# Kernel tuning notes

Measured on AMD Instinct MI355X. Metric: run time of the kernel, lower is better.

## Reference

```python
import jax, jax.numpy as jnp
import numpy as np

VOCAB, T, IN, H, L = 32000, 4096, 512, 256, 2


def setup_inputs() -> dict:
    key = jax.random.key(0)
    ks = jax.random.split(key, 32)
    inp = {}
    inp["tokens"] = jax.random.randint(ks[0], (T,), 0, VOCAB)
    inp["emb"] = jax.random.normal(ks[1], (VOCAB, IN), dtype=jnp.float32) * 0.02
    i = 2
    for d in ("f", "b"):
        for l in range(L):
            in_l = IN if l == 0 else H
            inp[f"{d}_Wih{l}"] = jax.random.normal(ks[i], (4 * H, in_l), dtype=jnp.float32) * 0.05; i += 1
            inp[f"{d}_Whh{l}"] = jax.random.normal(ks[i], (4 * H, H), dtype=jnp.float32) * 0.05; i += 1
            inp[f"{d}_bih{l}"] = jnp.zeros((4 * H,), dtype=jnp.float32)
            inp[f"{d}_bhh{l}"] = jnp.zeros((4 * H,), dtype=jnp.float32)
    return inp


def _lstm_layer(x_seq, Wih, Whh, bih, bhh):
    # x_seq: [T, in]; torch.nn.LSTMCell gate order: i, f, g, o
    Hh = Whh.shape[1]
    b = bih + bhh
    def step(carry, x):
        h, c = carry
        g = x @ Wih.T + h @ Whh.T + b           # [4H]
        i_, f_, g_, o_ = jnp.split(g, 4)
        c = jax.nn.sigmoid(f_) * c + jax.nn.sigmoid(i_) * jnp.tanh(g_)
        h = jax.nn.sigmoid(o_) * jnp.tanh(c)
        return (h, c), h
    z = jnp.zeros((Hh,), x_seq.dtype)
    (h, c), hs = jax.lax.scan(step, (z, z), x_seq)
    return hs, h, c                              # [T,H], [H], [H]


def _run_dir(x_seq, params):
    finals = []
    h_seq = x_seq
    for (Wih, Whh, bih, bhh) in params:
        h_seq, h, c = _lstm_layer(h_seq, Wih, Whh, bih, bhh)
        finals.append((c, h))
    return h_seq, finals


def reference(tokens, emb,
              f_Wih0, f_Whh0, f_bih0, f_bhh0, f_Wih1, f_Whh1, f_bih1, f_bhh1,
              b_Wih0, b_Whh0, b_bih0, b_bhh0, b_Wih1, b_Whh1, b_bih1, b_bhh1):
    x = emb[tokens]                              # [T, IN] embedding lookup
    fparams = [(f_Wih0, f_Whh0, f_bih0, f_bhh0), (f_Wih1, f_Whh1, f_bih1, f_bhh1)]
    bparams = [(b_Wih0, b_Whh0, b_bih0, b_bhh0), (b_Wih1, b_Whh1, b_bih1, b_bhh1)]
    f_out, f_fin = _run_dir(x, fparams)          # forward over sequence
    b_out_rev, b_fin = _run_dir(x[::-1], bparams)  # backward over reversed sequence
    b_out = b_out_rev[::-1]
    outputs = jnp.concatenate([f_out, b_out], axis=-1)  # [T, 2H]
    cell_memories = jnp.stack([jnp.stack([f_fin[l][0], b_fin[l][0]]) for l in range(L)])  # [L,2,H]
    hidden_states = jnp.stack([jnp.stack([f_fin[l][1], b_fin[l][1]]) for l in range(L)])  # [L,2,H]
    return cell_memories, hidden_states, outputs
```

## Files before the change

### kernel.cpp

```cpp
#include <hip/hip_runtime.h>
#include <math.h>

#define T_SEQ 4096

__device__ __forceinline__ float sigmoidf_(float x) {
  return 1.0f / (1.0f + expf(-x));
}

__device__ __forceinline__ unsigned long long pack_h(int tag, float h) {
  return ((unsigned long long)(unsigned)tag << 32) |
         (unsigned long long)__float_as_uint(h);
}

__global__ void gather_emb(const int* __restrict__ tokens,
                           const float4* __restrict__ emb4,
                           float4* __restrict__ X4) {
  int i = blockIdx.x * 256 + threadIdx.x;
  int t = i >> 7;
  int q = i & 127;
  X4[i] = emb4[(long)tokens[t] * 128 + q];
}

__global__ __launch_bounds__(256) void gemm_proj(
    const float* __restrict__ Xf, const float* __restrict__ Xb, int revb,
    const float* __restrict__ Wf, const float* __restrict__ Wb,
    const float* __restrict__ bihf, const float* __restrict__ bhhf,
    const float* __restrict__ bihb, const float* __restrict__ bhhb,
    float* __restrict__ Pf, float* __restrict__ Pb, int K)
{
  const int dirb = blockIdx.z;
  const float* X  = dirb ? Xb : Xf;
  const float* W  = dirb ? Wb : Wf;
  const float* bih = dirb ? bihb : bihf;
  const float* bhh = dirb ? bhhb : bhhf;
  float* Pp = dirb ? Pb : Pf;
  const int rev = dirb ? revb : 0;

  const int bn = blockIdx.x;
  const int bm = blockIdx.y;
  const int tid = threadIdx.x;
  const int tx = tid & 15, ty = tid >> 4;

  __shared__ float Xs[16][68];
  __shared__ float Ws[16][68];

  float acc[4][4] = {{0.f}};

  const int lrow = tid >> 2;
  const int lk4  = (tid & 3) * 4;
  const int xrow = bm * 64 + lrow;
  const int xsrc = rev ? (4095 - xrow) : xrow;
  const float* xptr = X + (long)xsrc * K + lk4;
  const float* wptr = W + (long)(bn * 64 + lrow) * K + lk4;

  for (int k0 = 0; k0 < K; k0 += 16) {
    float4 xv = *(const float4*)(xptr + k0);
    float4 wv = *(const float4*)(wptr + k0);
    __syncthreads();
    Xs[lk4 + 0][lrow] = xv.x; Xs[lk4 + 1][lrow] = xv.y;
    Xs[lk4 + 2][lrow] = xv.z; Xs[lk4 + 3][lrow] = xv.w;
    Ws[lk4 + 0][lrow] = wv.x; Ws[lk4 + 1][lrow] = wv.y;
    Ws[lk4 + 2][lrow] = wv.z; Ws[lk4 + 3][lrow] = wv.w;
    __syncthreads();
    #pragma unroll
    for (int kk = 0; kk < 16; ++kk) {
      float4 a = *(const float4*)(&Xs[kk][ty * 4]);
      float4 b = *(const float4*)(&Ws[kk][tx * 4]);
      acc[0][0] = fmaf(a.x, b.x, acc[0][0]); acc[0][1] = fmaf(a.x, b.y, acc[0][1]);
      acc[0][2] = fmaf(a.x, b.z, acc[0][2]); acc[0][3] = fmaf(a.x, b.w, acc[0][3]);
      acc[1][0] = fmaf(a.y, b.x, acc[1][0]); acc[1][1] = fmaf(a.y, b.y, acc[1][1]);
      acc[1][2] = fmaf(a.y, b.z, acc[1][2]); acc[1][3] = fmaf(a.y, b.w, acc[1][3]);
      acc[2][0] = fmaf(a.z, b.x, acc[2][0]); acc[2][1] = fmaf(a.z, b.y, acc[2][1]);
      acc[2][2] = fmaf(a.z, b.z, acc[2][2]); acc[2][3] = fmaf(a.z, b.w, acc[2][3]);
      acc[3][0] = fmaf(a.w, b.x, acc[3][0]); acc[3][1] = fmaf(a.w, b.y, acc[3][1]);
      acc[3][2] = fmaf(a.w, b.z, acc[3][2]); acc[3][3] = fmaf(a.w, b.w, acc[3][3]);
    }
  }

  const int c0 = bn * 64 + tx * 4;
  #pragma unroll
  for (int i = 0; i < 4; ++i) {
    const int r = bm * 64 + ty * 4 + i;
    float4 o4;
    o4.x = acc[i][0] + bih[c0 + 0] + bhh[c0 + 0];
    o4.y = acc[i][1] + bih[c0 + 1] + bhh[c0 + 1];
    o4.z = acc[i][2] + bih[c0 + 2] + bhh[c0 + 2];
    o4.w = acc[i][3] + bih[c0 + 3] + bhh[c0 + 3];
    *(float4*)(&Pp[(long)r * 1024 + c0]) = o4;
  }
}

__global__ __launch_bounds__(512, 2) void lstm_fused(
    const float* __restrict__ P0f, const float* __restrict__ P0b,
    const float* __restrict__ Whh0f, const float* __restrict__ Whh0b,
    const float* __restrict__ Wih1f, const float* __restrict__ Whh1f,
    const float* __restrict__ bih1f, const float* __restrict__ bhh1f,
    const float* __restrict__ Wih1b, const float* __restrict__ Whh1b,
    const float* __restrict__ bih1b, const float* __restrict__ bhh1b,
    float* __restrict__ out,
    unsigned long long* __restrict__ ring0,
    unsigned long long* __restrict__ h1x)
{
  const int bx = blockIdx.x;
  const int t  = threadIdx.x;

  __shared__ float hx[512];
  __shared__ float lds_c[64];
  __shared__ float part[8 * 264];

  if (t < 64) lds_c[t] = 0.0f;

  if (bx < 8) {
    const int d = bx >> 2, w = bx & 3;
    const float* __restrict__ P = d ? P0b : P0f;
    const float* __restrict__ W = d ? Whh0b : Whh0f;
    unsigned long long* ring = ring0 + (long)d * T_SEQ * 256;

    const int kb = t >> 6;
    const int jg = t & 63;

    float wreg[128];
    #pragma unroll
    for (int jj = 0; jj < 4; ++jj) {
      const int m = jg * 4 + jj;
      const int j = (m >> 6) * 256 + w * 64 + (m & 63);
      const float4* wrow = (const float4*)(W + (long)j * 256 + kb * 32);
      #pragma unroll
      for (int kq = 0; kq < 8; ++kq) {
        float4 v = wrow[kq];
        wreg[jj * 32 + kq * 4 + 0] = v.x;
        wreg[jj * 32 + kq * 4 + 1] = v.y;
        wreg[jj * 32 + kq * 4 + 2] = v.z;
        wreg[jj * 32 + kq * 4 + 3] = v.w;
      }
    }

    const int cell = w * 64 + (t & 63);
    const long pbase = (long)(t & 63) + w * 64;

    for (int s = 0; s < T_SEQ; ++s) {
      float p0 = 0.f, p1 = 0.f, p2 = 0.f, p3 = 0.f;
      if (t < 64) {
        const float* prow = P + (long)s * 1024 + pbase;
        p0 = prow[0]; p1 = prow[256]; p2 = prow[512]; p3 = prow[768];
      }

      if (s == 0) {
        if (t < 256) hx[t] = 0.0f;
      } else if (t < 256) {
        const unsigned long long* src = ring + (long)(s - 1) * 256 + t;
        unsigned long long v;
        do {
          v = __hip_atomic_load(src, __ATOMIC_RELAXED, __HIP_MEMORY_SCOPE_AGENT);
        } while ((unsigned)(v >> 32) != (unsigned)s);
        hx[t] = __uint_as_float((unsigned)v);
      }
      __syncthreads();

      float a0 = 0.f, a1 = 0.f, a2 = 0.f, a3 = 0.f;
      const float4* h4 = (const float4*)&hx[kb * 32];
      #pragma unroll
      for (int kq = 0; kq < 8; ++kq) {
        float4 hv = h4[kq];
        a0 = fmaf(wreg[0 * 32 + kq * 4 + 0], hv.x, a0);
        a0 = fmaf(wreg[0 * 32 + kq * 4 + 1], hv.y, a0);
        a0 = fmaf(wreg[0 * 32 + kq * 4 + 2], hv.z, a0);
        a0 = fmaf(wreg[0 * 32 + kq * 4 + 3], hv.w, a0);
        a1 = fmaf(wreg[1 * 32 + kq * 4 + 0], hv.x, a1);
        a1 = fmaf(wreg[1 * 32 + kq * 4 + 1], hv.y, a1);
        a1 = fmaf(wreg[1 * 32 + kq * 4 + 2], hv.z, a1);
        a1 = fmaf(wreg[1 * 32 + kq * 4 + 3], hv.w, a1);
        a2 = fmaf(wreg[2 * 32 + kq * 4 + 0], hv.x, a2);
        a2 = fmaf(wreg[2 * 32 + kq * 4 + 1], hv.y, a2);
        a2 = fmaf(wreg[2 * 32 + kq * 4 + 2], hv.z, a2);
        a2 = fmaf(wreg[2 * 32 + kq * 4 + 3], hv.w, a2);
        a3 = fmaf(wreg[3 * 32 + kq * 4 + 0], hv.x, a3);
        a3 = fmaf(wreg[3 * 32 + kq * 4 + 1], hv.y, a3);
        a3 = fmaf(wreg[3 * 32 + kq * 4 + 2], hv.z, a3);
        a3 = fmaf(wreg[3 * 32 + kq * 4 + 3], hv.w, a3);
      }
      float4 av; av.x = a0; av.y = a1; av.z = a2; av.w = a3;
      *(float4*)(&part[kb * 264 + jg * 4]) = av;
      __syncthreads();

      if (t < 64) {
        float s0 = p0, s1 = p1, s2 = p2, s3 = p3;
        #pragma unroll
        for (int q = 0; q < 8; ++q) {
          s0 += part[q * 264 + t];
          s1 += part[q * 264 + 64 + t];
          s2 += part[q * 264 + 128 + t];
          s3 += part[q * 264 + 192 + t];
        }
        float c = sigmoidf_(s1) * lds_c[t] + sigmoidf_(s0) * tanhf(s2);
        float h = sigmoidf_(s3) * tanhf(c);
        lds_c[t] = c;
        __hip_atomic_store(ring + (long)s * 256 + cell, pack_h(s + 1, h),
                           __ATOMIC_RELAXED, __HIP_MEMORY_SCOPE_AGENT);
        if (s == T_SEQ - 1) {
          out[d * 256 + cell] = c;
          out[1024 + d * 256 + cell] = h;
        }
      }
    }
  } else {
    const int i1 = bx - 8, d = i1 >> 3, w1 = i1 & 7;
    const float* __restrict__ Wih = d ? Wih1b : Wih1f;
    const float* __restrict__ Whh = d ? Whh1b : Whh1f;
    const float* __restrict__ bih = d ? bih1b : bih1f;
    const float* __restrict__ bhh = d ? bhh1b : bhh1f;
    unsigned long long* ring = ring0 + (long)d * T_SEQ * 256;
    unsigned long long* slot = h1x + d * 512;
    float* hout = d ? (out + 2048 + (long)4095 * 512 + 256) : (out + 2048);
    const long hstr = d ? -512 : 512;

    const int kb = t >> 6;
    const int jg = t & 63;

    float wreg[2][64];
    #pragma unroll
    for (int rr = 0; rr < 2; ++rr) {
      const int m = jg * 2 + rr;
      const int j = (m >> 5) * 256 + w1 * 32 + (m & 31);
      const float* srcw = (kb < 4) ? (Wih + (long)j * 256 + kb * 64)
                                   : (Whh + (long)j * 256 + (kb - 4) * 64);
      const float4* s4 = (const float4*)srcw;
      #pragma unroll
      for (int q = 0; q < 16; ++q) {
        float4 v = s4[q];
        wreg[rr][q * 4 + 0] = v.x; wreg[rr][q * 4 + 1] = v.y;
        wreg[rr][q * 4 + 2] = v.z; wreg[rr][q * 4 + 3] = v.w;
      }
    }

    const int cell = w1 * 32 + (t & 31);
    float b0 = 0.f, b1 = 0.f, b2 = 0.f, b3 = 0.f;
    if (t < 32) {
      b0 = bih[cell] + bhh[cell];
      b1 = bih[256 + cell] + bhh[256 + cell];
      b2 = bih[512 + cell] + bhh[512 + cell];
      b3 = bih[768 + cell] + bhh[768 + cell];
    }

    for (int s = 0; s < T_SEQ; ++s) {
      if (t < 256) {
        const unsigned long long* src = ring + (long)s * 256 + t;
        unsigned long long v;
        do {
          v = __hip_atomic_load(src, __ATOMIC_RELAXED, __HIP_MEMORY_SCOPE_AGENT);
        } while ((unsigned)(v >> 32) != (unsigned)(s + 1));
        hx[t] = __uint_as_float((unsigned)v);
      } else {
        const unsigned long long* src = slot + ((s + 1) & 1) * 256 + (t - 256);
        unsigned long long v;
        do {
          v = __hip_atomic_load(src, __ATOMIC_RELAXED, __HIP_MEMORY_SCOPE_AGENT);
        } while ((unsigned)(v >> 32) != (unsigned)s);
        hx[t] = __uint_as_float((unsigned)v);
      }
      __syncthreads();

      float a0 = 0.f, a1 = 0.f;
      const float4* h4 = (const float4*)&hx[kb * 64];
      #pragma unroll
      for (int q = 0; q < 16; ++q) {
        float4 hv = h4[q];
        a0 = fmaf(wreg[0][q * 4 + 0], hv.x, a0);
        a0 = fmaf(wreg[0][q * 4 + 1], hv.y, a0);
        a0 = fmaf(wreg[0][q * 4 + 2], hv.z, a0);
        a0 = fmaf(wreg[0][q * 4 + 3], hv.w, a0);
        a1 = fmaf(wreg[1][q * 4 + 0], hv.x, a1);
        a1 = fmaf(wreg[1][q * 4 + 1], hv.y, a1);
        a1 = fmaf(wreg[1][q * 4 + 2], hv.z, a1);
        a1 = fmaf(wreg[1][q * 4 + 3], hv.w, a1);
      }
      float2 av2; av2.x = a0; av2.y = a1;
      *(float2*)(&part[kb * 264 + jg * 2]) = av2;
      __syncthreads();

      if (t < 32) {
        float s0 = b0, s1 = b1, s2 = b2, s3 = b3;
        #pragma unroll
        for (int q = 0; q < 8; ++q) {
          s0 += part[q * 264 + t];
          s1 += part[q * 264 + 32 + t];
          s2 += part[q * 264 + 64 + t];
          s3 += part[q * 264 + 96 + t];
        }
        float c = sigmoidf_(s1) * lds_c[t] + sigmoidf_(s0) * tanhf(s2);
        float h = sigmoidf_(s3) * tanhf(c);
        lds_c[t] = c;
        __hip_atomic_store(&slot[(s & 1) * 256 + cell], pack_h(s + 1, h),
                           __ATOMIC_RELAXED, __HIP_MEMORY_SCOPE_AGENT);
        hout[(long)s * hstr + cell] = h;
        if (s == T_SEQ - 1) {
          out[512 + d * 256 + cell] = c;
          out[1024 + 512 + d * 256 + cell] = h;
        }
      }
    }
  }
}

extern "C" void kernel_launch(void* const* d_in, const int* in_sizes, int n_in,
                              void* d_out, int out_size, void* d_ws, size_t ws_size,
                              hipStream_t stream) {
  const int*   tokens = (const int*)d_in[0];
  const float* emb    = (const float*)d_in[1];
  const float* fWih0 = (const float*)d_in[2];
  const float* fWhh0 = (const float*)d_in[3];
  const float* fbih0 = (const float*)d_in[4];
  const float* fbhh0 = (const float*)d_in[5];
  const float* fWih1 = (const float*)d_in[6];
  const float* fWhh1 = (const float*)d_in[7];
  const float* fbih1 = (const float*)d_in[8];
  const float* fbhh1 = (const float*)d_in[9];
  const float* bWih0 = (const float*)d_in[10];
  const float* bWhh0 = (const float*)d_in[11];
  const float* bbih0 = (const float*)d_in[12];
  const float* bbhh0 = (const float*)d_in[13];
  const float* bWih1 = (const float*)d_in[14];
  const float* bWhh1 = (const float*)d_in[15];
  const float* bbih1 = (const float*)d_in[16];
  const float* bbhh1 = (const float*)d_in[17];

  float* out = (float*)d_out;
  float* ws  = (float*)d_ws;

  float* X   = ws;
  float* P0f = ws + 4194304;
  float* P0b = ws + 8388608;
  unsigned long long* ring0 = (unsigned long long*)ws;
  unsigned long long* h1x   = (unsigned long long*)(ws + 12582912);

  gather_emb<<<2048, 256, 0, stream>>>(tokens, (const float4*)emb, (float4*)X);

  gemm_proj<<<dim3(16, 64, 2), 256, 0, stream>>>(
      X, X, 1, fWih0, bWih0, fbih0, fbhh0, bbih0, bbhh0, P0f, P0b, 512);

  hipMemsetAsync(ring0, 0, (size_t)2 * T_SEQ * 256 * sizeof(unsigned long long), stream);
  hipMemsetAsync(h1x, 0, 1024 * sizeof(unsigned long long), stream);

  lstm_fused<<<dim3(24), 512, 0, stream>>>(
      P0f, P0b, fWhh0, bWhh0,
      fWih1, fWhh1, fbih1, fbhh1,
      bWih1, bWhh1, bbih1, bbhh1,
      out, ring0, h1x);
}
```

Baseline: 7.482 ms.

## Pin LSTM workgroups to two XCDs and use cache-bypass polling loads

The kernel now launches 512 workgroups. Each one reads its XCD id from a hardware register and claims one of 24 role slots through atomic CAS, so the forward direction lands on XCD 0 and the backward direction on XCD 1. Workgroups without a role exit, and the last arrivals take any slots still free. The handoff of hidden states between workgroups now uses inline-asm loads with sc0 (and sc0 sc1 every fourth poll) and a double store, replacing agent-scope relaxed atomics. The aim is to keep each direction's producers and consumers inside one XCD's shared L2 and cut cross-die latency on every step. The cost is launching and retiring many idle workgroups, plus reliance on cache-coherence bits whose exact behaviour is hardware-specific.

```diff
diff --git a/kernel.cpp b/kernel.cpp
--- a/kernel.cpp
+++ b/kernel.cpp
@@ -2,6 +2,7 @@
 #include <math.h>
 
 #define T_SEQ 4096
+#define NWG_LAUNCH 512
 
 __device__ __forceinline__ float sigmoidf_(float x) {
   return 1.0f / (1.0f + expf(-x));
@@ -10,6 +11,32 @@
 __device__ __forceinline__ unsigned long long pack_h(int tag, float h) {
   return ((unsigned long long)(unsigned)tag << 32) |
          (unsigned long long)__float_as_uint(h);
+}
+
+__device__ __forceinline__ unsigned long long ld_sc0(const unsigned long long* p) {
+  unsigned long long v;
+  asm volatile("global_load_dwordx2 %0, %1, off sc0\n\ts_waitcnt vmcnt(0)"
+               : "=v"(v) : "v"(p) : "memory");
+  return v;
+}
+__device__ __forceinline__ unsigned long long ld_mall(const unsigned long long* p) {
+  unsigned long long v;
+  asm volatile("global_load_dwordx2 %0, %1, off sc0 sc1\n\ts_waitcnt vmcnt(0)"
+               : "=v"(v) : "v"(p) : "memory");
+  return v;
+}
+__device__ __forceinline__ void st_pub(unsigned long long* p, unsigned long long v) {
+  asm volatile("global_store_dwordx2 %0, %1, off sc0\n\t"
+               "global_store_dwordx2 %0, %1, off sc0 sc1"
+               :: "v"(p), "v"(v) : "memory");
+}
+__device__ __forceinline__ float poll_h(const unsigned long long* p, unsigned want) {
+  int it = 0;
+  for (;;) {
+    unsigned long long v = ((it & 3) == 3) ? ld_mall(p) : ld_sc0(p);
+    if ((unsigned)(v >> 32) == want) return __uint_as_float((unsigned)v);
+    ++it;
+  }
 }
 
 __global__ void gather_emb(const int* __restrict__ tokens,
@@ -99,10 +126,35 @@
     const float* __restrict__ bih1b, const float* __restrict__ bhh1b,
     float* __restrict__ out,
     unsigned long long* __restrict__ ring0,
-    unsigned long long* __restrict__ h1x)
+    unsigned long long* __restrict__ h1x,
+    int* __restrict__ flags)
 {
-  const int bx = blockIdx.x;
-  const int t  = threadIdx.x;
+  const int t = threadIdx.x;
+
+  __shared__ int role_s;
+  if (t == 0) {
+    int xcd;
+    asm volatile("s_getreg_b32 %0, hwreg(20, 0, 32)" : "=s"(xcd));
+    xcd &= 7;
+    int role = -1;
+    const int lo = (xcd == 0) ? 0 : (xcd == 1 ? 12 : -1);
+    if (lo >= 0) {
+      for (int r = lo; r < lo + 12 && role < 0; ++r)
+        if (atomicCAS(&flags[r], 0, 1) == 0) role = r;
+    }
+    const int n = atomicAdd(&flags[24], 1) + 1;
+    if (role < 0 && n > NWG_LAUNCH - 32) {
+      for (int r = 0; r < 24 && role < 0; ++r)
+        if (atomicCAS(&flags[r], 0, 1) == 0) role = r;
+    }
+    role_s = role;
+  }
+  __syncthreads();
+  const int role = role_s;
+  if (role < 0) return;
+
+  const int d   = role < 12 ? 0 : 1;
+  const int sub = role < 12 ? role : role - 12;
 
   __shared__ float hx[512];
   __shared__ float lds_c[64];
@@ -110,11 +162,12 @@
 
   if (t < 64) lds_c[t] = 0.0f;
 
-  if (bx < 8) {
-    const int d = bx >> 2, w = bx & 3;
+  unsigned long long* ring = ring0 + (long)d * T_SEQ * 256;
+
+  if (sub < 4) {
+    const int w = sub;
     const float* __restrict__ P = d ? P0b : P0f;
     const float* __restrict__ W = d ? Whh0b : Whh0f;
-    unsigned long long* ring = ring0 + (long)d * T_SEQ * 256;
 
     const int kb = t >> 6;
     const int jg = t & 63;
@@ -148,12 +201,7 @@
       if (s == 0) {
         if (t < 256) hx[t] = 0.0f;
       } else if (t < 256) {
-        const unsigned long long* src = ring + (long)(s - 1) * 256 + t;
-        unsigned long long v;
-        do {
-          v = __hip_atomic_load(src, __ATOMIC_RELAXED, __HIP_MEMORY_SCOPE_AGENT);
-        } while ((unsigned)(v >> 32) != (unsigned)s);
-        hx[t] = __uint_as_float((unsigned)v);
+        hx[t] = poll_h(ring + (long)(s - 1) * 256 + t, (unsigned)s);
       }
       __syncthreads();
 
@@ -195,8 +243,7 @@
         float c = sigmoidf_(s1) * lds_c[t] + sigmoidf_(s0) * tanhf(s2);
         float h = sigmoidf_(s3) * tanhf(c);
         lds_c[t] = c;
-        __hip_atomic_store(ring + (long)s * 256 + cell, pack_h(s + 1, h),
-                           __ATOMIC_RELAXED, __HIP_MEMORY_SCOPE_AGENT);
+        st_pub(ring + (long)s * 256 + cell, pack_h(s + 1, h));
         if (s == T_SEQ - 1) {
           out[d * 256 + cell] = c;
           out[1024 + d * 256 + cell] = h;
@@ -204,12 +251,11 @@
       }
     }
   } else {
-    const int i1 = bx - 8, d = i1 >> 3, w1 = i1 & 7;
+    const int w1 = sub - 4;
     const float* __restrict__ Wih = d ? Wih1b : Wih1f;
     const float* __restrict__ Whh = d ? Whh1b : Whh1f;
     const float* __restrict__ bih = d ? bih1b : bih1f;
     const float* __restrict__ bhh = d ? bhh1b : bhh1f;
-    unsigned long long* ring = ring0 + (long)d * T_SEQ * 256;
     unsigned long long* slot = h1x + d * 512;
     float* hout = d ? (out + 2048 + (long)4095 * 512 + 256) : (out + 2048);
     const long hstr = d ? -512 : 512;
@@ -244,19 +290,9 @@
 
     for (int s = 0; s < T_SEQ; ++s) {
       if (t < 256) {
-        const unsigned long long* src = ring + (long)s * 256 + t;
-        unsigned long long v;
-        do {
-          v = __hip_atomic_load(src, __ATOMIC_RELAXED, __HIP_MEMORY_SCOPE_AGENT);
-        } while ((unsigned)(v >> 32) != (unsigned)(s + 1));
-        hx[t] = __uint_as_float((unsigned)v);
+        hx[t] = poll_h(ring + (long)s * 256 + t, (unsigned)(s + 1));
       } else {
-        const unsigned long long* src = slot + ((s + 1) & 1) * 256 + (t - 256);
-        unsigned long long v;
-        do {
-          v = __hip_atomic_load(src, __ATOMIC_RELAXED, __HIP_MEMORY_SCOPE_AGENT);
-        } while ((unsigned)(v >> 32) != (unsigned)s);
-        hx[t] = __uint_as_float((unsigned)v);
+        hx[t] = poll_h(slot + ((s + 1) & 1) * 256 + (t - 256), (unsigned)s);
       }
       __syncthreads();
 
@@ -290,8 +326,7 @@
         float c = sigmoidf_(s1) * lds_c[t] + sigmoidf_(s0) * tanhf(s2);
         float h = sigmoidf_(s3) * tanhf(c);
         lds_c[t] = c;
-        __hip_atomic_store(&slot[(s & 1) * 256 + cell], pack_h(s + 1, h),
-                           __ATOMIC_RELAXED, __HIP_MEMORY_SCOPE_AGENT);
+        st_pub(&slot[(s & 1) * 256 + cell], pack_h(s + 1, h));
         hout[(long)s * hstr + cell] = h;
         if (s == T_SEQ - 1) {
           out[512 + d * 256 + cell] = c;
@@ -332,6 +367,7 @@
   float* P0b = ws + 8388608;
   unsigned long long* ring0 = (unsigned long long*)ws;
   unsigned long long* h1x   = (unsigned long long*)(ws + 12582912);
+  int* flags = (int*)(ws + 12584960);
 
   gather_emb<<<2048, 256, 0, stream>>>(tokens, (const float4*)emb, (float4*)X);
 
@@ -339,11 +375,11 @@
       X, X, 1, fWih0, bWih0, fbih0, fbhh0, bbih0, bbhh0, P0f, P0b, 512);
 
   hipMemsetAsync(ring0, 0, (size_t)2 * T_SEQ * 256 * sizeof(unsigned long long), stream);
-  hipMemsetAsync(h1x, 0, 1024 * sizeof(unsigned long long), stream);
-
-  lstm_fused<<<dim3(24), 512, 0, stream>>>(
+  hipMemsetAsync(h1x, 0, 1024 * sizeof(unsigned long long) + 32 * sizeof(int), stream);
+
+  lstm_fused<<<dim3(NWG_LAUNCH), 512, 0, stream>>>(
       P0f, P0b, fWhh0, bWhh0,
       fWih1, fWhh1, fbih1, fbhh1,
       bWih1, bWhh1, bbih1, bbhh1,
-      out, ring0, h1x);
-}
+      out, ring0, h1x, flags);
+}
```

Measured after the change: 7.026 ms. -6.1%, faster.

## Parallelize gate activations across threads and use inline-asm cache-bypassing poll/publish

Applied to the files above, without the earlier changes.

Two changes to the persistent recurrent LSTM kernel. Gate reduction and activation now run across 256 (layer 0) or 128 (layer 1) threads, one gate per thread, written to a new shared gact buffer. Only the cell update stays on 64/32 threads. This costs an extra __syncthreads per step in exchange for a shorter serial transcendental chain. The relaxed atomic loads and stores on the inter-block h exchange are replaced with inline-asm global loads and stores carrying sc0 sc1 cache bits, with two loads in flight per poll iteration. This aims to cut the per-step handoff latency, but it depends on MI300-family ISA cache-control semantics being correct for coherence.

```diff
diff --git a/kernel.cpp b/kernel.cpp
--- a/kernel.cpp
+++ b/kernel.cpp
@@ -10,6 +10,27 @@
 __device__ __forceinline__ unsigned long long pack_h(int tag, float h) {
   return ((unsigned long long)(unsigned)tag << 32) |
          (unsigned long long)__float_as_uint(h);
+}
+
+__device__ __forceinline__ void st_pub(unsigned long long* p, unsigned long long v) {
+  asm volatile("global_store_dwordx2 %0, %1, off sc0 sc1"
+               :: "v"(p), "v"(v) : "memory");
+}
+
+__device__ __forceinline__ float poll_h(const unsigned long long* p, unsigned want) {
+  for (;;) {
+    unsigned long long a, b;
+    asm volatile("global_load_dwordx2 %0, %2, off sc0 sc1\n\t"
+                 "global_load_dwordx2 %1, %2, off sc0 sc1\n\t"
+                 "s_waitcnt vmcnt(1)"
+                 : "=&v"(a), "=&v"(b) : "v"(p) : "memory");
+    if ((unsigned)(a >> 32) == want) {
+      asm volatile("s_waitcnt vmcnt(0)" ::: "memory");
+      return __uint_as_float((unsigned)a);
+    }
+    asm volatile("s_waitcnt vmcnt(0)" ::: "memory");
+    if ((unsigned)(b >> 32) == want) return __uint_as_float((unsigned)b);
+  }
 }
 
 __global__ void gather_emb(const int* __restrict__ tokens,
@@ -105,8 +126,9 @@
   const int t  = threadIdx.x;
 
   __shared__ float hx[512];
+  __shared__ float part[8 * 264];
+  __shared__ float gact[256];
   __shared__ float lds_c[64];
-  __shared__ float part[8 * 264];
 
   if (t < 64) lds_c[t] = 0.0f;
 
@@ -135,25 +157,17 @@
       }
     }
 
-    const int cell = w * 64 + (t & 63);
-    const long pbase = (long)(t & 63) + w * 64;
+    const long pj   = (long)((t >> 6) * 256 + w * 64 + (t & 63));
+    const int  cell = w * 64 + (t & 63);
 
     for (int s = 0; s < T_SEQ; ++s) {
-      float p0 = 0.f, p1 = 0.f, p2 = 0.f, p3 = 0.f;
-      if (t < 64) {
-        const float* prow = P + (long)s * 1024 + pbase;
-        p0 = prow[0]; p1 = prow[256]; p2 = prow[512]; p3 = prow[768];
-      }
+      float pval = 0.0f;
+      if (t < 256) pval = P[(long)s * 1024 + pj];
 
       if (s == 0) {
         if (t < 256) hx[t] = 0.0f;
       } else if (t < 256) {
-        const unsigned long long* src = ring + (long)(s - 1) * 256 + t;
-        unsigned long long v;
-        do {
-          v = __hip_atomic_load(src, __ATOMIC_RELAXED, __HIP_MEMORY_SCOPE_AGENT);
-        } while ((unsigned)(v >> 32) != (unsigned)s);
-        hx[t] = __uint_as_float((unsigned)v);
+        hx[t] = poll_h(ring + (long)(s - 1) * 256 + t, (unsigned)s);
       }
       __syncthreads();
 
@@ -183,20 +197,19 @@
       *(float4*)(&part[kb * 264 + jg * 4]) = av;
       __syncthreads();
 
+      if (t < 256) {
+        float g = pval;
+        #pragma unroll
+        for (int q = 0; q < 8; ++q) g += part[q * 264 + t];
+        gact[t] = ((t >> 6) == 2) ? tanhf(g) : sigmoidf_(g);
+      }
+      __syncthreads();
+
       if (t < 64) {
-        float s0 = p0, s1 = p1, s2 = p2, s3 = p3;
-        #pragma unroll
-        for (int q = 0; q < 8; ++q) {
-          s0 += part[q * 264 + t];
-          s1 += part[q * 264 + 64 + t];
-          s2 += part[q * 264 + 128 + t];
-          s3 += part[q * 264 + 192 + t];
-        }
-        float c = sigmoidf_(s1) * lds_c[t] + sigmoidf_(s0) * tanhf(s2);
-        float h = sigmoidf_(s3) * tanhf(c);
+        float c = gact[64 + t] * lds_c[t] + gact[t] * gact[128 + t];
+        float h = gact[192 + t] * tanhf(c);
         lds_c[t] = c;
-        __hip_atomic_store(ring + (long)s * 256 + cell, pack_h(s + 1, h),
-                           __ATOMIC_RELAXED, __HIP_MEMORY_SCOPE_AGENT);
+        st_pub(ring + (long)s * 256 + cell, pack_h(s + 1, h));
         if (s == T_SEQ - 1) {
           out[d * 256 + cell] = c;
           out[1024 + d * 256 + cell] = h;
@@ -234,29 +247,17 @@
     }
 
     const int cell = w1 * 32 + (t & 31);
-    float b0 = 0.f, b1 = 0.f, b2 = 0.f, b3 = 0.f;
-    if (t < 32) {
-      b0 = bih[cell] + bhh[cell];
-      b1 = bih[256 + cell] + bhh[256 + cell];
-      b2 = bih[512 + cell] + bhh[512 + cell];
-      b3 = bih[768 + cell] + bhh[768 + cell];
+    float bsum = 0.0f;
+    if (t < 128) {
+      const int j = (t >> 5) * 256 + w1 * 32 + (t & 31);
+      bsum = bih[j] + bhh[j];
     }
 
     for (int s = 0; s < T_SEQ; ++s) {
       if (t < 256) {
-        const unsigned long long* src = ring + (long)s * 256 + t;
-        unsigned long long v;
-        do {
-          v = __hip_atomic_load(src, __ATOMIC_RELAXED, __HIP_MEMORY_SCOPE_AGENT);
-        } while ((unsigned)(v >> 32) != (unsigned)(s + 1));
-        hx[t] = __uint_as_float((unsigned)v);
+        hx[t] = poll_h(ring + (long)s * 256 + t, (unsigned)(s + 1));
       } else {
-        const unsigned long long* src = slot + ((s + 1) & 1) * 256 + (t - 256);
-        unsigned long long v;
-        do {
-          v = __hip_atomic_load(src, __ATOMIC_RELAXED, __HIP_MEMORY_SCOPE_AGENT);
-        } while ((unsigned)(v >> 32) != (unsigned)s);
-        hx[t] = __uint_as_float((unsigned)v);
+        hx[t] = poll_h(slot + ((s + 1) & 1) * 256 + (t - 256), (unsigned)s);
       }
       __syncthreads();
 
@@ -278,20 +279,19 @@
       *(float2*)(&part[kb * 264 + jg * 2]) = av2;
       __syncthreads();
 
+      if (t < 128) {
+        float g = bsum;
+        #pragma unroll
+        for (int q = 0; q < 8; ++q) g += part[q * 264 + t];
+        gact[t] = ((t >> 5) == 2) ? tanhf(g) : sigmoidf_(g);
+      }
+      __syncthreads();
+
       if (t < 32) {
-        float s0 = b0, s1 = b1, s2 = b2, s3 = b3;
-        #pragma unroll
-        for (int q = 0; q < 8; ++q) {
-          s0 += part[q * 264 + t];
-          s1 += part[q * 264 + 32 + t];
-          s2 += part[q * 264 + 64 + t];
-          s3 += part[q * 264 + 96 + t];
-        }
-        float c = sigmoidf_(s1) * lds_c[t] + sigmoidf_(s0) * tanhf(s2);
-        float h = sigmoidf_(s3) * tanhf(c);
+        float c = gact[32 + t] * lds_c[t] + gact[t] * gact[64 + t];
+        float h = gact[96 + t] * tanhf(c);
         lds_c[t] = c;
-        __hip_atomic_store(&slot[(s & 1) * 256 + cell], pack_h(s + 1, h),
-                           __ATOMIC_RELAXED, __HIP_MEMORY_SCOPE_AGENT);
+        st_pub(&slot[(s & 1) * 256 + cell], pack_h(s + 1, h));
         hout[(long)s * hstr + cell] = h;
         if (s == T_SEQ - 1) {
           out[512 + d * 256 + cell] = c;
```

After: 7.346 ms. Within noise of the previous version (-1.8%).
